# Optimization experiments

Hardware: AMD Instinct MI355X
Metric: run time of the kernel (lower is better)

## Reference

```python
import jax, jax.numpy as jnp
import numpy as np

N = 250000          # number of points (also used as padded #unique voxels)
EPS = 1e-5          # BatchNorm1d eps
DIMS = [9, 64, 128, 256, 64]
PROJ = 16


def _bn(x, g, b):
    # torch BatchNorm1d in training mode: biased batch var
    m = jnp.mean(x, axis=0)
    v = jnp.var(x, axis=0)
    return (x - m) * jax.lax.rsqrt(v + EPS) * g + b


def setup_inputs() -> dict:
    key = jax.random.key(0)
    ks = list(jax.random.split(key, 24))
    inp = {
        "feats": jax.random.normal(ks[0], (N, DIMS[0]), jnp.float32),
        "coords": jax.random.randint(ks[1], (N, 3), 0, 48, jnp.int32),
    }
    k = 2
    # 4 BatchNorms over dims 9, 64, 128, 256
    for i, d in enumerate(DIMS[:4]):
        inp[f"bn{i}_g"] = jnp.ones((d,), jnp.float32)
        inp[f"bn{i}_b"] = jnp.zeros((d,), jnp.float32)
    # 4 Linear layers 9->64->128->256->64, stored as [in, out]
    for i in range(4):
        fin, fout = DIMS[i], DIMS[i + 1]
        inp[f"w{i+1}"] = jax.random.normal(ks[k], (fin, fout), jnp.float32) * (1.0 / np.sqrt(fin)); k += 1
        inp[f"b{i+1}"] = jnp.zeros((fout,), jnp.float32)
    # feature projection 64 -> 16 (kaiming-ish init, bias 0.01)
    inp["wp"] = jax.random.normal(ks[k], (DIMS[4], PROJ), jnp.float32) * np.sqrt(2.0 / PROJ); k += 1
    inp["bp"] = jnp.full((PROJ,), 0.01, jnp.float32)
    return inp


def reference(feats, coords, bn0_g, bn0_b, bn1_g, bn1_b, bn2_g, bn2_b, bn3_g, bn3_b,
              w1, b1, w2, b2, w3, b3, w4, b4, wp, bp):
    # unique voxel coords (sorted rows, like torch.unique dim=0); padded to N for jit
    unq, inv, cnt = jnp.unique(coords, axis=0, return_inverse=True, return_counts=True,
                               size=N, fill_value=-1)
    inv = inv.reshape(-1)

    # point MLP: BN -> Lin -> BN -> ReLU -> Lin -> BN -> ReLU -> Lin -> BN -> ReLU -> Lin
    x = _bn(feats, bn0_g, bn0_b)
    x = jax.nn.relu(_bn(x @ w1 + b1, bn1_g, bn1_b))
    x = jax.nn.relu(_bn(x @ w2 + b2, bn2_g, bn2_b))
    x = jax.nn.relu(_bn(x @ w3 + b3, bn3_g, bn3_b))
    x = x @ w4 + b4                                   # [N, 64]

    # scatter_max pooling per voxel; empty (padding) segments zeroed
    pooled = jax.ops.segment_max(x, inv, num_segments=N)
    pooled = jnp.where((cnt > 0)[:, None], pooled, 0.0)

    # feature projection + ReLU
    pooled = jax.nn.relu(pooled @ wp + bp)            # [N, 16] (rows >= #unique are padding)
    return pooled, unq.astype(jnp.int32)
```

## Files before the change

kernel.cpp:

```cpp
#include <hip/hip_runtime.h>
#include <hip/hip_bf16.h>

#define EPSBN 1e-5f
#define NKEYS 110592
#define SLICES 64

typedef __attribute__((ext_vector_type(8))) short bf16x8;
typedef __attribute__((ext_vector_type(4))) float f32x4;

__device__ __forceinline__ unsigned fmap(float f){
  unsigned u = __float_as_uint(f);
  return (u & 0x80000000u) ? ~u : (u | 0x80000000u);
}
__device__ __forceinline__ float funmap(unsigned k){
  unsigned u = (k & 0x80000000u) ? (k & 0x7fffffffu) : ~k;
  return __uint_as_float(u);
}
__device__ __forceinline__ float bf2f(ushort u){ return __uint_as_float(((unsigned)u)<<16); }
__device__ __forceinline__ ushort f2bf(float f){
  unsigned u = __float_as_uint(f);
  unsigned r = u + 0x7fffu + ((u>>16)&1u);
  return (ushort)(r>>16);
}

template<int KP>
__device__ __forceinline__ int swz(int row, int kbyte){
  constexpr int MASK = (KP >= 64) ? 7 : 3;
  return row*(KP*2) + (kbyte ^ ((row & MASK) << 4));
}

__device__ __forceinline__ int tri(int k, int l){
  if (k > l){ int t=k; k=l; l=t; }
  return k*9 - (k*(k-1))/2 + (l-k);
}

__global__ __launch_bounds__(256) void k_zero(uint4* __restrict__ p, size_t n16){
  size_t i = (size_t)blockIdx.x*256 + threadIdx.x;
  size_t stride = (size_t)gridDim.x*256;
  uint4 z = make_uint4(0,0,0,0);
  for (; i < n16; i += stride) p[i] = z;
}

__global__ __launch_bounds__(256) void k_wprep(const float* __restrict__ w,
    ushort* __restrict__ wf, int K, int M){
  int CT = M >> 4;
  int KS = (K + 31) >> 5;
  int total = KS*CT*512;
  for (int idx = blockIdx.x*256 + threadIdx.x; idx < total; idx += gridDim.x*256){
    int e = idx & 7, l = (idx>>3) & 63, c = idx >> 9;
    int ct = c % CT, ks = c / CT;
    int g = l >> 4, j = l & 15;
    int k = ks*32 + g*8 + e, col = ct*16 + j;
    wf[idx] = (k < K) ? f2bf(w[(size_t)k*M + col]) : (ushort)0;
  }
}

__global__ __launch_bounds__(256) void k_keys(const int* __restrict__ coords,
    unsigned* __restrict__ cnt, int n){
  int i = blockIdx.x*256 + threadIdx.x;
  if (i >= n) return;
  int x = coords[3*i+0], y = coords[3*i+1], z = coords[3*i+2];
  atomicAdd(&cnt[(unsigned)((x*48 + y)*48 + z)], 1u);
}

__global__ __launch_bounds__(256) void k_scan1(const unsigned* __restrict__ cnt,
    unsigned* __restrict__ rloc, unsigned* __restrict__ bsum){
  __shared__ unsigned ts[256];
  int t = threadIdx.x;
  int base = blockIdx.x*1024 + t*4;
  uint4 cv = *(const uint4*)&cnt[base];
  unsigned v0 = cv.x?1u:0u, v1 = cv.y?1u:0u, v2 = cv.z?1u:0u, v3 = cv.w?1u:0u;
  unsigned s = v0+v1+v2+v3;
  ts[t] = s;
  __syncthreads();
  for (int off=1; off<256; off<<=1){
    unsigned add = (t>=off) ? ts[t-off] : 0u;
    __syncthreads();
    ts[t] += add;
    __syncthreads();
  }
  unsigned run = ts[t] - s;
  rloc[base+0] = run; run += v0;
  rloc[base+1] = run; run += v1;
  rloc[base+2] = run; run += v2;
  rloc[base+3] = run;
  if (t == 255) bsum[blockIdx.x] = ts[255];
}

__global__ __launch_bounds__(128) void k_scan2(const unsigned* __restrict__ bsum,
    unsigned* __restrict__ boff){
  __shared__ unsigned ts[128];
  int t = threadIdx.x;
  unsigned v = (t < 108) ? bsum[t] : 0u;
  ts[t] = v;
  __syncthreads();
  for (int off=1; off<128; off<<=1){
    unsigned add = (t>=off) ? ts[t-off] : 0u;
    __syncthreads();
    ts[t] += add;
    __syncthreads();
  }
  boff[t] = ts[t] - v;
}

__global__ __launch_bounds__(256) void k_unq(const unsigned* __restrict__ cnt,
    const unsigned* __restrict__ rloc, const unsigned* __restrict__ boff,
    float* __restrict__ unq){
  int k = blockIdx.x*256 + threadIdx.x;
  if (k >= NKEYS) return;
  if (cnt[k] == 0) return;
  unsigned r = rloc[k] + boff[k>>10];
  float z = (float)(k % 48);
  float y = (float)((k/48) % 48);
  float x = (float)(k / 2304);
  unq[3*(size_t)r+0] = x; unq[3*(size_t)r+1] = y; unq[3*(size_t)r+2] = z;
}

__global__ __launch_bounds__(256) void k_pad(const unsigned* __restrict__ boff,
    float* __restrict__ unq, int n){
  int i = blockIdx.x*256 + threadIdx.x;
  if (i >= n) return;
  if ((unsigned)i >= boff[108]){
    unq[3*(size_t)i+0] = -1.f; unq[3*(size_t)i+1] = -1.f; unq[3*(size_t)i+2] = -1.f;
  }
}

__global__ __launch_bounds__(256) void k_inv(const int* __restrict__ coords,
    const unsigned* __restrict__ rloc, const unsigned* __restrict__ boff,
    unsigned* __restrict__ inv, int n){
  int i = blockIdx.x*256 + threadIdx.x;
  if (i >= n) return;
  int x = coords[3*i+0], y = coords[3*i+1], z = coords[3*i+2];
  unsigned k = (unsigned)((x*48 + y)*48 + z);
  inv[i] = rloc[k] + boff[k>>10];
}

__global__ __launch_bounds__(256) void k_stats0x(const float* __restrict__ X,
    float* __restrict__ slices, int n){
  float s[9], q[45];
  #pragma unroll
  for (int k=0;k<9;k++) s[k]=0.f;
  #pragma unroll
  for (int i=0;i<45;i++) q[i]=0.f;
  int stride = gridDim.x*256;
  for (int i = blockIdx.x*256 + threadIdx.x; i < n; i += stride){
    float v[9];
    #pragma unroll
    for (int k=0;k<9;k++) v[k] = X[(size_t)i*9+k];
    int qi=0;
    #pragma unroll
    for (int k=0;k<9;k++){
      s[k] += v[k];
      #pragma unroll
      for (int l=k;l<9;l++) q[qi++] += v[k]*v[l];
    }
  }
  #pragma unroll
  for (int off=32; off>0; off>>=1){
    #pragma unroll
    for (int k=0;k<9;k++)  s[k] += __shfl_down(s[k], off, 64);
    #pragma unroll
    for (int i=0;i<45;i++) q[i] += __shfl_down(q[i], off, 64);
  }
  if ((threadIdx.x & 63) == 0){
    float* sl = slices + (size_t)(blockIdx.x & (SLICES-1))*54;
    #pragma unroll
    for (int k=0;k<9;k++)  atomicAdd(&sl[k],   s[k]);
    #pragma unroll
    for (int i=0;i<45;i++) atomicAdd(&sl[9+i], q[i]);
  }
}

__global__ void k_fin01(const float* __restrict__ slices, float invN,
    const float* __restrict__ g0, const float* __restrict__ b0,
    const float* __restrict__ g1, const float* __restrict__ b1,
    const float* __restrict__ w1, float* __restrict__ ac0, float* __restrict__ ac1){
  __shared__ float red[54];
  int t = threadIdx.x;
  if (t < 54){
    float a = 0.f;
    for (int sl=0; sl<SLICES; sl++) a += slices[(size_t)sl*54 + t];
    red[t] = a;
  }
  __syncthreads();
  float m[9], a0[9], c0[9], qb[45];
  #pragma unroll
  for (int k=0;k<9;k++) m[k] = red[k]*invN;
  #pragma unroll
  for (int i=0;i<45;i++) qb[i] = red[9+i]*invN;
  #pragma unroll
  for (int k=0;k<9;k++){
    float var = qb[tri(k,k)] - m[k]*m[k];
    a0[k] = g0[k]*rsqrtf(var + EPSBN);
    c0[k] = b0[k] - m[k]*a0[k];
  }
  if (t < 9){ ac0[t] = a0[t]; ac0[9+t] = c0[t]; }
  float wj[9];
  #pragma unroll
  for (int k=0;k<9;k++) wj[k] = w1[(size_t)k*64 + t];
  float mean = 0.f;
  #pragma unroll
  for (int k=0;k<9;k++) mean += (m[k]*a0[k] + c0[k])*wj[k];
  float e2 = 0.f;
  #pragma unroll
  for (int k=0;k<9;k++)
    #pragma unroll
    for (int l=0;l<9;l++){
      float U = a0[k]*a0[l]*qb[tri(k,l)] + a0[k]*c0[l]*m[k] + a0[l]*c0[k]*m[l] + c0[k]*c0[l];
      e2 += wj[k]*wj[l]*U;
    }
  float var = e2 - mean*mean;
  float a = g1[t]*rsqrtf(var + EPSBN);
  ac1[t] = a;
  ac1[64+t] = b1[t] - mean*a;
}

__global__ void k_fin(const float* __restrict__ slices, int M, float invN,
    const float* __restrict__ g, const float* __restrict__ b, float* __restrict__ ac){
  int j = blockIdx.x*64 + threadIdx.x;
  if (j >= M) return;
  float s = 0.f, ss = 0.f;
  for (int sl = 0; sl < SLICES; sl++){
    s  += slices[(size_t)sl*2*M + j];
    ss += slices[(size_t)sl*2*M + M + j];
  }
  float mean = s*invN;
  float var = ss*invN - mean*mean;
  float a = g[j]*rsqrtf(var + EPSBN);
  ac[j] = a;
  ac[M+j] = b[j] - mean*a;
}

template<int DEPTH>
__global__ __launch_bounds__(256,2) void k_chain(
    const float* __restrict__ feats, const float* __restrict__ ac0,
    const ushort* __restrict__ w1f, const float* __restrict__ ac1,
    const ushort* __restrict__ w2f, const float* __restrict__ ac2,
    const ushort* __restrict__ w3f, const float* __restrict__ ac3,
    const ushort* __restrict__ w4f, const float* __restrict__ b4,
    const unsigned* __restrict__ inv, unsigned* __restrict__ pooled,
    float* __restrict__ slices, int n){
  constexpr int SMEM = (DEPTH==2) ? 12288 : (DEPTH==3) ? 28672 : 32768;
  __shared__ __align__(16) char smem[SMEM];
  char* X0 = smem;

  int t = threadIdx.x;
  int lane = t & 63, w = t >> 6;
  int lrow = lane & 15, lgrp = lane >> 4;
  int rowbase = blockIdx.x * 64;

  bf16x8 b1 = *(const bf16x8*)(w1f + (size_t)(w*64 + lane)*8);

  for (int e = t; e < 2048; e += 256){
    int row = e >> 5, k = e & 31;
    int gr = rowbase + row;
    float v = (k < 9 && gr < n) ? fmaf(feats[(size_t)gr*9 + k], ac0[k], ac0[9+k]) : 0.f;
    *(ushort*)(X0 + swz<32>(row, k*2)) = f2bf(v);
  }
  __syncthreads();

  f32x4 acc0[4] = {};
  #pragma unroll
  for (int rb = 0; rb < 4; rb++){
    bf16x8 a = *(const bf16x8*)(X0 + swz<32>(rb*16 + lrow, lgrp*16));
    acc0[rb] = __builtin_amdgcn_mfma_f32_16x16x32_bf16(a, b1, acc0[rb], 0,0,0);
  }

  char* T1 = smem + 4096;
  {
    int j = w*16 + lrow;
    float a1 = ac1[j], c1 = ac1[64+j];
    #pragma unroll
    for (int rb=0;rb<4;rb++)
      #pragma unroll
      for (int r=0;r<4;r++){
        int row = rb*16 + 4*lgrp + r;
        float v = fmaxf(fmaf(acc0[rb][r], a1, c1), 0.f);
        if (rowbase + row >= n) v = 0.f;
        *(ushort*)(T1 + swz<64>(row, j*2)) = f2bf(v);
      }
  }
  __syncthreads();

  f32x4 acc1[4][2] = {};
  #pragma unroll
  for (int ks=0; ks<2; ks++){
    bf16x8 bb[2];
    #pragma unroll
    for (int f=0;f<2;f++)
      bb[f] = *(const bf16x8*)(w2f + (size_t)((ks*8 + 2*w + f)*64 + lane)*8);
    #pragma unroll
    for (int rb=0;rb<4;rb++){
      bf16x8 a = *(const bf16x8*)(T1 + swz<64>(rb*16 + lrow, ks*64 + lgrp*16));
      #pragma unroll
      for (int f=0;f<2;f++)
        acc1[rb][f] = __builtin_amdgcn_mfma_f32_16x16x32_bf16(a, bb[f], acc1[rb][f], 0,0,0);
    }
  }

  if constexpr (DEPTH == 2){
    float s[2]={0.f,0.f}, ss[2]={0.f,0.f};
    #pragma unroll
    for (int rb=0;rb<4;rb++)
      #pragma unroll
      for (int f=0;f<2;f++)
        #pragma unroll
        for (int r=0;r<4;r++){ float v=acc1[rb][f][r]; s[f]+=v; ss[f]+=v*v; }
    __syncthreads();
    float* ssum = (float*)smem;
    ssum[t] = 0.f;
    __syncthreads();
    #pragma unroll
    for (int f=0;f<2;f++){
      int j = w*32 + 16*f + lrow;
      atomicAdd(&ssum[j], s[f]); atomicAdd(&ssum[128+j], ss[f]);
    }
    __syncthreads();
    float* gsl = slices + (size_t)(blockIdx.x & (SLICES-1))*256;
    atomicAdd(&gsl[t], ssum[t]);
    return;
  }

  if constexpr (DEPTH >= 3){
  char* T2 = smem + 12288;
  #pragma unroll
  for (int f=0;f<2;f++){
    int j = w*32 + 16*f + lrow;
    float a2 = ac2[j], c2 = ac2[128+j];
    #pragma unroll
    for (int rb=0;rb<4;rb++)
      #pragma unroll
      for (int r=0;r<4;r++){
        int row = rb*16 + 4*lgrp + r;
        float v = fmaxf(fmaf(acc1[rb][f][r], a2, c2), 0.f);
        if (rowbase + row >= n) v = 0.f;
        *(ushort*)(T2 + swz<128>(row, j*2)) = f2bf(v);
      }
  }
  __syncthreads();

  if constexpr (DEPTH == 3){
    float s3[2][2], ss3[2][2];
    #pragma unroll
    for (int h=0; h<2; h++){
      f32x4 acc2[4][2] = {};
      #pragma unroll
      for (int ks=0; ks<4; ks++){
        bf16x8 bb[2];
        #pragma unroll
        for (int f=0;f<2;f++)
          bb[f] = *(const bf16x8*)(w3f + (size_t)((ks*16 + 4*w + 2*h + f)*64 + lane)*8);
        #pragma unroll
        for (int rb=0;rb<4;rb++){
          bf16x8 a = *(const bf16x8*)(T2 + swz<128>(rb*16 + lrow, ks*64 + lgrp*16));
          #pragma unroll
          for (int f=0;f<2;f++)
            acc2[rb][f] = __builtin_amdgcn_mfma_f32_16x16x32_bf16(a, bb[f], acc2[rb][f], 0,0,0);
        }
      }
      #pragma unroll
      for (int f=0;f<2;f++){
        float s=0.f, ss=0.f;
        #pragma unroll
        for (int rb=0;rb<4;rb++)
          #pragma unroll
          for (int r=0;r<4;r++){ float v=acc2[rb][f][r]; s+=v; ss+=v*v; }
        s3[h][f]=s; ss3[h][f]=ss;
      }
    }
    __syncthreads();
    float* ssum = (float*)smem;
    for (int e=t; e<512; e+=256) ssum[e] = 0.f;
    __syncthreads();
    #pragma unroll
    for (int h=0;h<2;h++)
      #pragma unroll
      for (int f=0;f<2;f++){
        int j = 64*w + 32*h + 16*f + lrow;
        atomicAdd(&ssum[j], s3[h][f]); atomicAdd(&ssum[256+j], ss3[h][f]);
      }
    __syncthreads();
    float* gsl = slices + (size_t)(blockIdx.x & (SLICES-1))*512;
    for (int e=t; e<512; e+=256) atomicAdd(&gsl[e], ssum[e]);
    return;
  }

  if constexpr (DEPTH == 4){
  f32x4 acc2[4][4] = {};
  #pragma unroll
  for (int ks=0; ks<4; ks++){
    bf16x8 bb[4];
    #pragma unroll
    for (int f=0;f<4;f++)
      bb[f] = *(const bf16x8*)(w3f + (size_t)((ks*16 + 4*w + f)*64 + lane)*8);
    #pragma unroll
    for (int rb=0;rb<4;rb++){
      bf16x8 a = *(const bf16x8*)(T2 + swz<128>(rb*16 + lrow, ks*64 + lgrp*16));
      #pragma unroll
      for (int f=0;f<4;f++)
        acc2[rb][f] = __builtin_amdgcn_mfma_f32_16x16x32_bf16(a, bb[f], acc2[rb][f], 0,0,0);
    }
  }
  __syncthreads();

  char* X3 = smem;
  #pragma unroll
  for (int f=0;f<4;f++){
    int j = 64*w + 16*f + lrow;
    float a3 = ac3[j], c3 = ac3[256+j];
    #pragma unroll
    for (int rb=0;rb<4;rb++)
      #pragma unroll
      for (int r=0;r<4;r++){
        int row = rb*16 + 4*lgrp + r;
        float v = fmaxf(fmaf(acc2[rb][f][r], a3, c3), 0.f);
        if (rowbase + row >= n) v = 0.f;
        *(ushort*)(X3 + swz<256>(row, j*2)) = f2bf(v);
      }
  }
  __syncthreads();

  f32x4 acc3[4] = {};
  #pragma unroll
  for (int ks=0; ks<8; ks++){
    bf16x8 b = *(const bf16x8*)(w4f + (size_t)((ks*4 + w)*64 + lane)*8);
    #pragma unroll
    for (int rb=0;rb<4;rb++){
      bf16x8 a = *(const bf16x8*)(X3 + swz<256>(rb*16 + lrow, ks*64 + lgrp*16));
      acc3[rb] = __builtin_amdgcn_mfma_f32_16x16x32_bf16(a, b, acc3[rb], 0,0,0);
    }
  }

  {
    int j = w*16 + lrow;
    float bias4 = b4[j];
    #pragma unroll
    for (int rb=0;rb<4;rb++)
      #pragma unroll
      for (int r=0;r<4;r++){
        int gr = rowbase + 16*rb + 4*lgrp + r;
        if (gr < n){
          unsigned seg = inv[gr];
          atomicMax(&pooled[(size_t)seg*64 + j], fmap(acc3[rb][r] + bias4));
        }
      }
  }
  }
  }
}

__global__ __launch_bounds__(256) void k_proj(const unsigned* __restrict__ pooled,
    const float* __restrict__ wp, const float* __restrict__ bp,
    const unsigned* __restrict__ boff, float* __restrict__ out, int n){
  __shared__ float wps[64][16];
  __shared__ float pl[16][66];
  int t = threadIdx.x;
  for (int e=t; e<1024; e+=256) wps[e>>4][e&15] = wp[e];
  unsigned M = boff[108];
  int rowbase = blockIdx.x*16;
  #pragma unroll
  for (int p=0;p<4;p++){
    int e = t + p*256;
    int r = e >> 6, k = e & 63;
    int gr = rowbase + r;
    float f = 0.f;
    if (gr < (int)M) f = funmap(pooled[(size_t)gr*64 + k]);
    pl[r][k] = f;
  }
  __syncthreads();
  int r = t >> 4, j = t & 15;
  int gr = rowbase + r;
  if (gr < n){
    float acc = bp[j];
    #pragma unroll
    for (int k=0;k<64;k++) acc = fmaf(pl[r][k], wps[k][j], acc);
    out[(size_t)gr*16 + j] = fmaxf(acc, 0.f);
  }
}

extern "C" void kernel_launch(void* const* d_in, const int* in_sizes, int n_in,
                              void* d_out, int out_size, void* d_ws, size_t ws_size,
                              hipStream_t stream){
  (void)n_in; (void)out_size;
  const float* feats  = (const float*)d_in[0];
  const int*   coords = (const int*)d_in[1];
  const float* g0=(const float*)d_in[2];  const float* bb0=(const float*)d_in[3];
  const float* g1=(const float*)d_in[4];  const float* bb1=(const float*)d_in[5];
  const float* g2=(const float*)d_in[6];  const float* bb2=(const float*)d_in[7];
  const float* g3=(const float*)d_in[8];  const float* bb3=(const float*)d_in[9];
  const float* w1=(const float*)d_in[10]; const float* b1=(const float*)d_in[11];
  const float* w2=(const float*)d_in[12];
  const float* w3=(const float*)d_in[14];
  const float* w4=(const float*)d_in[16]; const float* b4=(const float*)d_in[17];
  const float* wp=(const float*)d_in[18]; const float* bp=(const float*)d_in[19];
  (void)b1;
  int n = in_sizes[0]/9;

  char* ws = (char*)d_ws;
  size_t off = 0;
  auto alloc = [&](size_t bytes){ size_t o = off; off = (off + bytes + 255) & ~(size_t)255; return o; };
  size_t o_cnt  = alloc((size_t)NKEYS*4);
  size_t o_sl0  = alloc((size_t)SLICES*54*4);
  size_t o_sl2  = alloc((size_t)SLICES*256*4);
  size_t o_sl3  = alloc((size_t)SLICES*512*4);
  size_t zero_end = off;
  size_t o_rloc = alloc((size_t)NKEYS*4);
  size_t o_bsum = alloc(128*4);
  size_t o_boff = alloc(128*4);
  size_t o_ac0  = alloc(18*4);
  size_t o_ac1  = alloc(128*4);
  size_t o_ac2  = alloc(256*4);
  size_t o_ac3  = alloc(512*4);
  size_t o_w1f  = alloc(2048*2);
  size_t o_w2f  = alloc(8192*2);
  size_t o_w3f  = alloc(32768*2);
  size_t o_w4f  = alloc(16384*2);
  size_t o_inv  = alloc((size_t)n*4);
  size_t npool = (n < NKEYS ? (size_t)n : (size_t)NKEYS);
  size_t pool_bytes = npool*64*4;
  size_t o_pool = alloc(pool_bytes);
  if (ws_size < off) return;

  unsigned* cnt  = (unsigned*)(ws + o_cnt);
  unsigned* rloc = (unsigned*)(ws + o_rloc);
  unsigned* bsum = (unsigned*)(ws + o_bsum);
  unsigned* boff = (unsigned*)(ws + o_boff);
  unsigned* inv  = (unsigned*)(ws + o_inv);
  float* sl0 = (float*)(ws + o_sl0);
  float* sl2 = (float*)(ws + o_sl2);
  float* sl3 = (float*)(ws + o_sl3);
  float* ac0 = (float*)(ws + o_ac0);
  float* ac1 = (float*)(ws + o_ac1);
  float* ac2 = (float*)(ws + o_ac2);
  float* ac3 = (float*)(ws + o_ac3);
  ushort* w1f = (ushort*)(ws + o_w1f);
  ushort* w2f = (ushort*)(ws + o_w2f);
  ushort* w3f = (ushort*)(ws + o_w3f);
  ushort* w4f = (ushort*)(ws + o_w4f);
  unsigned* pooled = (unsigned*)(ws + o_pool);

  float* out_pool = (float*)d_out;
  float* out_unq  = out_pool + (size_t)n*16;

  {
    size_t n16 = zero_end/16;
    int zb = (int)((n16 + 255)/256); if (zb > 2048) zb = 2048;
    k_zero<<<zb,256,0,stream>>>((uint4*)ws, n16);
  }
  {
    size_t n16 = pool_bytes/16;
    int zb = (int)((n16 + 255)/256); if (zb > 2048) zb = 2048;
    k_zero<<<zb,256,0,stream>>>((uint4*)(ws + o_pool), n16);
  }

  k_wprep<<<8,256,0,stream>>>(w1, w1f, 9, 64);
  k_wprep<<<32,256,0,stream>>>(w2, w2f, 64, 128);
  k_wprep<<<128,256,0,stream>>>(w3, w3f, 128, 256);
  k_wprep<<<64,256,0,stream>>>(w4, w4f, 256, 64);

  int nb = (n + 255)/256;
  k_keys<<<nb,256,0,stream>>>(coords, cnt, n);
  k_scan1<<<NKEYS/1024,256,0,stream>>>(cnt, rloc, bsum);
  k_scan2<<<1,128,0,stream>>>(bsum, boff);
  k_unq<<<(NKEYS+255)/256,256,0,stream>>>(cnt, rloc, boff, out_unq);
  k_pad<<<nb,256,0,stream>>>(boff, out_unq, n);
  k_inv<<<nb,256,0,stream>>>(coords, rloc, boff, inv, n);

  k_stats0x<<<512,256,0,stream>>>(feats, sl0, n);
  k_fin01<<<1,64,0,stream>>>(sl0, 1.f/(float)n, g0, bb0, g1, bb1, w1, ac0, ac1);

  int gb = (n+63)/64;
  k_chain<2><<<gb,256,0,stream>>>(feats, ac0, w1f, ac1, w2f, ac2, w3f, ac3, w4f, b4, inv, pooled, sl2, n);
  k_fin<<<2,64,0,stream>>>(sl2, 128, 1.f/(float)n, g2, bb2, ac2);

  k_chain<3><<<gb,256,0,stream>>>(feats, ac0, w1f, ac1, w2f, ac2, w3f, ac3, w4f, b4, inv, pooled, sl3, n);
  k_fin<<<4,64,0,stream>>>(sl3, 256, 1.f/(float)n, g3, bb3, ac3);

  k_chain<4><<<gb,256,0,stream>>>(feats, ac0, w1f, ac1, w2f, ac2, w3f, ac3, w4f, b4, inv, pooled, nullptr, n);

  k_proj<<<(n+15)/16,256,0,stream>>>(pooled, wp, bp, boff, out_pool, n);
}
```

Measured before the change: 334.7 us.

## Replace atomicMax scatter pooling with CSR gather pooling over bf16 activations

The final MLP stage now writes bf16 per-point outputs to a buffer instead of doing per-element atomicMax into a zeroed pooled array. A second scan over voxel counts and a cursor-based CSR fill are added, so a new pooling kernel can gather each voxel's points, take the max per channel and apply the projection in one pass. This removes the atomics and the pooled-buffer zeroing, at the cost of an extra n*64 bf16 write and read, random gathers, and bf16 rounding of the pre-pool activations.

```diff
diff --git a/kernel.cpp b/kernel.cpp
--- a/kernel.cpp
+++ b/kernel.cpp
@@ -8,14 +8,6 @@
 typedef __attribute__((ext_vector_type(8))) short bf16x8;
 typedef __attribute__((ext_vector_type(4))) float f32x4;
 
-__device__ __forceinline__ unsigned fmap(float f){
-  unsigned u = __float_as_uint(f);
-  return (u & 0x80000000u) ? ~u : (u | 0x80000000u);
-}
-__device__ __forceinline__ float funmap(unsigned k){
-  unsigned u = (k & 0x80000000u) ? (k & 0x7fffffffu) : ~k;
-  return __uint_as_float(u);
-}
 __device__ __forceinline__ float bf2f(ushort u){ return __uint_as_float(((unsigned)u)<<16); }
 __device__ __forceinline__ ushort f2bf(float f){
   unsigned u = __float_as_uint(f);
@@ -64,75 +56,86 @@
 }
 
 __global__ __launch_bounds__(256) void k_scan1(const unsigned* __restrict__ cnt,
-    unsigned* __restrict__ rloc, unsigned* __restrict__ bsum){
-  __shared__ unsigned ts[256];
+    unsigned* __restrict__ rloc, unsigned* __restrict__ ploc, unsigned* __restrict__ bsum){
+  __shared__ unsigned tf[256], tc[256];
   int t = threadIdx.x;
   int base = blockIdx.x*1024 + t*4;
   uint4 cv = *(const uint4*)&cnt[base];
-  unsigned v0 = cv.x?1u:0u, v1 = cv.y?1u:0u, v2 = cv.z?1u:0u, v3 = cv.w?1u:0u;
-  unsigned s = v0+v1+v2+v3;
-  ts[t] = s;
+  unsigned f0 = cv.x?1u:0u, f1 = cv.y?1u:0u, f2 = cv.z?1u:0u, f3 = cv.w?1u:0u;
+  unsigned sf = f0+f1+f2+f3;
+  unsigned sc = cv.x+cv.y+cv.z+cv.w;
+  tf[t] = sf; tc[t] = sc;
   __syncthreads();
   for (int off=1; off<256; off<<=1){
-    unsigned add = (t>=off) ? ts[t-off] : 0u;
-    __syncthreads();
-    ts[t] += add;
-    __syncthreads();
-  }
-  unsigned run = ts[t] - s;
-  rloc[base+0] = run; run += v0;
-  rloc[base+1] = run; run += v1;
-  rloc[base+2] = run; run += v2;
-  rloc[base+3] = run;
-  if (t == 255) bsum[blockIdx.x] = ts[255];
+    unsigned af = (t>=off) ? tf[t-off] : 0u;
+    unsigned ac = (t>=off) ? tc[t-off] : 0u;
+    __syncthreads();
+    tf[t] += af; tc[t] += ac;
+    __syncthreads();
+  }
+  unsigned rf = tf[t] - sf, rc = tc[t] - sc;
+  rloc[base+0] = rf; rf += f0;    ploc[base+0] = rc; rc += cv.x;
+  rloc[base+1] = rf; rf += f1;    ploc[base+1] = rc; rc += cv.y;
+  rloc[base+2] = rf; rf += f2;    ploc[base+2] = rc; rc += cv.z;
+  rloc[base+3] = rf;              ploc[base+3] = rc;
+  if (t == 255){ bsum[2*blockIdx.x] = tf[255]; bsum[2*blockIdx.x+1] = tc[255]; }
 }
 
 __global__ __launch_bounds__(128) void k_scan2(const unsigned* __restrict__ bsum,
     unsigned* __restrict__ boff){
-  __shared__ unsigned ts[128];
+  __shared__ unsigned tf[128], tc[128];
   int t = threadIdx.x;
-  unsigned v = (t < 108) ? bsum[t] : 0u;
-  ts[t] = v;
+  unsigned vf = (t < 108) ? bsum[2*t] : 0u;
+  unsigned vc = (t < 108) ? bsum[2*t+1] : 0u;
+  tf[t] = vf; tc[t] = vc;
   __syncthreads();
   for (int off=1; off<128; off<<=1){
-    unsigned add = (t>=off) ? ts[t-off] : 0u;
-    __syncthreads();
-    ts[t] += add;
-    __syncthreads();
-  }
-  boff[t] = ts[t] - v;
+    unsigned af = (t>=off) ? tf[t-off] : 0u;
+    unsigned ac = (t>=off) ? tc[t-off] : 0u;
+    __syncthreads();
+    tf[t] += af; tc[t] += ac;
+    __syncthreads();
+  }
+  boff[2*t] = tf[t] - vf;
+  boff[2*t+1] = tc[t] - vc;
 }
 
 __global__ __launch_bounds__(256) void k_unq(const unsigned* __restrict__ cnt,
-    const unsigned* __restrict__ rloc, const unsigned* __restrict__ boff,
-    float* __restrict__ unq){
+    const unsigned* __restrict__ rloc, const unsigned* __restrict__ ploc,
+    const unsigned* __restrict__ boff, float* __restrict__ unq,
+    unsigned* __restrict__ vst, unsigned* __restrict__ vct){
   int k = blockIdx.x*256 + threadIdx.x;
   if (k >= NKEYS) return;
-  if (cnt[k] == 0) return;
-  unsigned r = rloc[k] + boff[k>>10];
+  unsigned c = cnt[k];
+  if (c == 0) return;
+  unsigned r  = rloc[k] + boff[2*(k>>10)];
+  unsigned st = ploc[k] + boff[2*(k>>10)+1];
   float z = (float)(k % 48);
   float y = (float)((k/48) % 48);
   float x = (float)(k / 2304);
   unq[3*(size_t)r+0] = x; unq[3*(size_t)r+1] = y; unq[3*(size_t)r+2] = z;
+  vst[r] = st; vct[r] = c;
 }
 
 __global__ __launch_bounds__(256) void k_pad(const unsigned* __restrict__ boff,
     float* __restrict__ unq, int n){
   int i = blockIdx.x*256 + threadIdx.x;
   if (i >= n) return;
-  if ((unsigned)i >= boff[108]){
+  if ((unsigned)i >= boff[216]){
     unq[3*(size_t)i+0] = -1.f; unq[3*(size_t)i+1] = -1.f; unq[3*(size_t)i+2] = -1.f;
   }
 }
 
-__global__ __launch_bounds__(256) void k_inv(const int* __restrict__ coords,
-    const unsigned* __restrict__ rloc, const unsigned* __restrict__ boff,
-    unsigned* __restrict__ inv, int n){
+__global__ __launch_bounds__(256) void k_csr(const int* __restrict__ coords,
+    const unsigned* __restrict__ ploc, const unsigned* __restrict__ boff,
+    unsigned* __restrict__ cursor, unsigned* __restrict__ csr, int n){
   int i = blockIdx.x*256 + threadIdx.x;
   if (i >= n) return;
   int x = coords[3*i+0], y = coords[3*i+1], z = coords[3*i+2];
   unsigned k = (unsigned)((x*48 + y)*48 + z);
-  inv[i] = rloc[k] + boff[k>>10];
+  unsigned slot = atomicAdd(&cursor[k], 1u);
+  unsigned st = ploc[k] + boff[2*(k>>10)+1];
+  csr[st + slot] = i;
 }
 
 __global__ __launch_bounds__(256) void k_stats0x(const float* __restrict__ X,
@@ -238,8 +241,7 @@
     const ushort* __restrict__ w2f, const float* __restrict__ ac2,
     const ushort* __restrict__ w3f, const float* __restrict__ ac3,
     const ushort* __restrict__ w4f, const float* __restrict__ b4,
-    const unsigned* __restrict__ inv, unsigned* __restrict__ pooled,
-    float* __restrict__ slices, int n){
+    ushort* __restrict__ y4, float* __restrict__ slices, int n){
   constexpr int SMEM = (DEPTH==2) ? 12288 : (DEPTH==3) ? 28672 : 32768;
   __shared__ __align__(16) char smem[SMEM];
   char* X0 = smem;
@@ -439,42 +441,50 @@
       #pragma unroll
       for (int r=0;r<4;r++){
         int gr = rowbase + 16*rb + 4*lgrp + r;
-        if (gr < n){
-          unsigned seg = inv[gr];
-          atomicMax(&pooled[(size_t)seg*64 + j], fmap(acc3[rb][r] + bias4));
-        }
-      }
-  }
-  }
-  }
-}
-
-__global__ __launch_bounds__(256) void k_proj(const unsigned* __restrict__ pooled,
+        if (gr < n) y4[(size_t)gr*64 + j] = f2bf(acc3[rb][r] + bias4);
+      }
+  }
+  }
+  }
+}
+
+__global__ __launch_bounds__(256) void k_pool(const ushort* __restrict__ y4,
+    const unsigned* __restrict__ csr, const unsigned* __restrict__ vst,
+    const unsigned* __restrict__ vct, const unsigned* __restrict__ boff,
     const float* __restrict__ wp, const float* __restrict__ bp,
-    const unsigned* __restrict__ boff, float* __restrict__ out, int n){
-  __shared__ float wps[64][16];
-  __shared__ float pl[16][66];
-  int t = threadIdx.x;
-  for (int e=t; e<1024; e+=256) wps[e>>4][e&15] = wp[e];
-  unsigned M = boff[108];
-  int rowbase = blockIdx.x*16;
-  #pragma unroll
-  for (int p=0;p<4;p++){
-    int e = t + p*256;
-    int r = e >> 6, k = e & 63;
-    int gr = rowbase + r;
-    float f = 0.f;
-    if (gr < (int)M) f = funmap(pooled[(size_t)gr*64 + k]);
-    pl[r][k] = f;
-  }
-  __syncthreads();
-  int r = t >> 4, j = t & 15;
-  int gr = rowbase + r;
-  if (gr < n){
-    float acc = bp[j];
-    #pragma unroll
-    for (int k=0;k<64;k++) acc = fmaf(pl[r][k], wps[k][j], acc);
-    out[(size_t)gr*16 + j] = fmaxf(acc, 0.f);
+    float* __restrict__ out, int n){
+  __shared__ float wps[1024];
+  __shared__ float sm[4][64];
+  int t = threadIdx.x, w = t >> 6, lane = t & 63;
+  for (int e=t; e<1024; e+=256) wps[e] = wp[e];
+  int r = blockIdx.x*4 + w;
+  unsigned M = boff[216];
+  if (r < n){
+    float m;
+    if (r < (int)M){
+      unsigned st = vst[r], c = vct[r];
+      unsigned nc = c < 64u ? c : 64u;
+      unsigned pi_l = (lane < nc) ? csr[st + lane] : 0u;
+      m = -__builtin_inff();
+      for (unsigned p=0; p<nc; p++){
+        unsigned pi = __shfl(pi_l, (int)p, 64);
+        m = fmaxf(m, bf2f(y4[(size_t)pi*64 + lane]));
+      }
+      for (unsigned p=nc; p<c; p++){
+        unsigned pi = csr[st + p];
+        m = fmaxf(m, bf2f(y4[(size_t)pi*64 + lane]));
+      }
+    } else {
+      m = 0.f;
+    }
+    sm[w][lane] = m;
+  }
+  __syncthreads();
+  if (r < n && lane < 16){
+    float acc = bp[lane];
+    #pragma unroll 8
+    for (int j=0; j<64; j++) acc = fmaf(sm[w][j], wps[j*16 + lane], acc);
+    out[(size_t)r*16 + lane] = fmaxf(acc, 0.f);
   }
 }
 
@@ -488,25 +498,26 @@
   const float* g1=(const float*)d_in[4];  const float* bb1=(const float*)d_in[5];
   const float* g2=(const float*)d_in[6];  const float* bb2=(const float*)d_in[7];
   const float* g3=(const float*)d_in[8];  const float* bb3=(const float*)d_in[9];
-  const float* w1=(const float*)d_in[10]; const float* b1=(const float*)d_in[11];
+  const float* w1=(const float*)d_in[10];
   const float* w2=(const float*)d_in[12];
   const float* w3=(const float*)d_in[14];
   const float* w4=(const float*)d_in[16]; const float* b4=(const float*)d_in[17];
   const float* wp=(const float*)d_in[18]; const float* bp=(const float*)d_in[19];
-  (void)b1;
   int n = in_sizes[0]/9;
 
   char* ws = (char*)d_ws;
   size_t off = 0;
   auto alloc = [&](size_t bytes){ size_t o = off; off = (off + bytes + 255) & ~(size_t)255; return o; };
   size_t o_cnt  = alloc((size_t)NKEYS*4);
+  size_t o_cur  = alloc((size_t)NKEYS*4);
   size_t o_sl0  = alloc((size_t)SLICES*54*4);
   size_t o_sl2  = alloc((size_t)SLICES*256*4);
   size_t o_sl3  = alloc((size_t)SLICES*512*4);
   size_t zero_end = off;
   size_t o_rloc = alloc((size_t)NKEYS*4);
-  size_t o_bsum = alloc(128*4);
-  size_t o_boff = alloc(128*4);
+  size_t o_ploc = alloc((size_t)NKEYS*4);
+  size_t o_bsum = alloc(256*4);
+  size_t o_boff = alloc(256*4);
   size_t o_ac0  = alloc(18*4);
   size_t o_ac1  = alloc(128*4);
   size_t o_ac2  = alloc(256*4);
@@ -515,17 +526,18 @@
   size_t o_w2f  = alloc(8192*2);
   size_t o_w3f  = alloc(32768*2);
   size_t o_w4f  = alloc(16384*2);
-  size_t o_inv  = alloc((size_t)n*4);
-  size_t npool = (n < NKEYS ? (size_t)n : (size_t)NKEYS);
-  size_t pool_bytes = npool*64*4;
-  size_t o_pool = alloc(pool_bytes);
+  size_t o_csr  = alloc((size_t)n*4);
+  size_t o_vst  = alloc((size_t)n*4);
+  size_t o_vct  = alloc((size_t)n*4);
+  size_t o_y4   = alloc((size_t)n*64*2);
   if (ws_size < off) return;
 
   unsigned* cnt  = (unsigned*)(ws + o_cnt);
+  unsigned* cursor = (unsigned*)(ws + o_cur);
   unsigned* rloc = (unsigned*)(ws + o_rloc);
+  unsigned* ploc = (unsigned*)(ws + o_ploc);
   unsigned* bsum = (unsigned*)(ws + o_bsum);
   unsigned* boff = (unsigned*)(ws + o_boff);
-  unsigned* inv  = (unsigned*)(ws + o_inv);
   float* sl0 = (float*)(ws + o_sl0);
   float* sl2 = (float*)(ws + o_sl2);
   float* sl3 = (float*)(ws + o_sl3);
@@ -537,7 +549,10 @@
   ushort* w2f = (ushort*)(ws + o_w2f);
   ushort* w3f = (ushort*)(ws + o_w3f);
   ushort* w4f = (ushort*)(ws + o_w4f);
-  unsigned* pooled = (unsigned*)(ws + o_pool);
+  unsigned* csr = (unsigned*)(ws + o_csr);
+  unsigned* vst = (unsigned*)(ws + o_vst);
+  unsigned* vct = (unsigned*)(ws + o_vct);
+  ushort* y4 = (ushort*)(ws + o_y4);
 
   float* out_pool = (float*)d_out;
   float* out_unq  = out_pool + (size_t)n*16;
@@ -547,11 +562,6 @@
     int zb = (int)((n16 + 255)/256); if (zb > 2048) zb = 2048;
     k_zero<<<zb,256,0,stream>>>((uint4*)ws, n16);
   }
-  {
-    size_t n16 = pool_bytes/16;
-    int zb = (int)((n16 + 255)/256); if (zb > 2048) zb = 2048;
-    k_zero<<<zb,256,0,stream>>>((uint4*)(ws + o_pool), n16);
-  }
 
   k_wprep<<<8,256,0,stream>>>(w1, w1f, 9, 64);
   k_wprep<<<32,256,0,stream>>>(w2, w2f, 64, 128);
@@ -560,23 +570,23 @@
 
   int nb = (n + 255)/256;
   k_keys<<<nb,256,0,stream>>>(coords, cnt, n);
-  k_scan1<<<NKEYS/1024,256,0,stream>>>(cnt, rloc, bsum);
+  k_scan1<<<NKEYS/1024,256,0,stream>>>(cnt, rloc, ploc, bsum);
   k_scan2<<<1,128,0,stream>>>(bsum, boff);
-  k_unq<<<(NKEYS+255)/256,256,0,stream>>>(cnt, rloc, boff, out_unq);
+  k_unq<<<(NKEYS+255)/256,256,0,stream>>>(cnt, rloc, ploc, boff, out_unq, vst, vct);
   k_pad<<<nb,256,0,stream>>>(boff, out_unq, n);
-  k_inv<<<nb,256,0,stream>>>(coords, rloc, boff, inv, n);
+  k_csr<<<nb,256,0,stream>>>(coords, ploc, boff, cursor, csr, n);
 
   k_stats0x<<<512,256,0,stream>>>(feats, sl0, n);
   k_fin01<<<1,64,0,stream>>>(sl0, 1.f/(float)n, g0, bb0, g1, bb1, w1, ac0, ac1);
 
   int gb = (n+63)/64;
-  k_chain<2><<<gb,256,0,stream>>>(feats, ac0, w1f, ac1, w2f, ac2, w3f, ac3, w4f, b4, inv, pooled, sl2, n);
+  k_chain<2><<<gb,256,0,stream>>>(feats, ac0, w1f, ac1, w2f, ac2, w3f, ac3, w4f, b4, nullptr, sl2, n);
   k_fin<<<2,64,0,stream>>>(sl2, 128, 1.f/(float)n, g2, bb2, ac2);
 
-  k_chain<3><<<gb,256,0,stream>>>(feats, ac0, w1f, ac1, w2f, ac2, w3f, ac3, w4f, b4, inv, pooled, sl3, n);
+  k_chain<3><<<gb,256,0,stream>>>(feats, ac0, w1f, ac1, w2f, ac2, w3f, ac3, w4f, b4, nullptr, sl3, n);
   k_fin<<<4,64,0,stream>>>(sl3, 256, 1.f/(float)n, g3, bb3, ac3);
 
-  k_chain<4><<<gb,256,0,stream>>>(feats, ac0, w1f, ac1, w2f, ac2, w3f, ac3, w4f, b4, inv, pooled, nullptr, n);
-
-  k_proj<<<(n+15)/16,256,0,stream>>>(pooled, wp, bp, boff, out_pool, n);
-}
+  k_chain<4><<<gb,256,0,stream>>>(feats, ac0, w1f, ac1, w2f, ac2, w3f, ac3, w4f, b4, y4, nullptr, n);
+
+  k_pool<<<(n+3)/4,256,0,stream>>>(y4, csr, vst, vct, boff, wp, bp, out_pool, n);
+}
```

Result: slower. 382.9 us (+14.4%).
